# Performance work log

Measured on AMD Instinct MI355X. Metric: run time of the kernel, lower is better.

The kernel has to match this reference:

```python
import jax, jax.numpy as jnp
import numpy as np

B, T, C = 64, 256, 384
H, D = 6, 64  # num_heads, head_size

def setup_inputs() -> dict:
    key = jax.random.key(0)
    ks = jax.random.split(key, 6)
    s = 0.02
    return {
        "x": jax.random.normal(ks[0], (B, T, C), dtype=jnp.float32),
        "Wq": jax.random.normal(ks[1], (H, C, D), dtype=jnp.float32) * s,
        "Wk": jax.random.normal(ks[2], (H, C, D), dtype=jnp.float32) * s,
        "Wv": jax.random.normal(ks[3], (H, C, D), dtype=jnp.float32) * s,
        "Wp": jax.random.normal(ks[4], (C, C), dtype=jnp.float32) * s,
        "bp": jnp.zeros((C,), dtype=jnp.float32),
    }

def reference(x, Wq, Wk, Wv, Wp, bp):
    # per-head projections: [B,T,C] x [H,C,D] -> [B,H,T,D]
    q = jnp.einsum('btc,hcd->bhtd', x, Wq)
    k = jnp.einsum('btc,hcd->bhtd', x, Wk)
    v = jnp.einsum('btc,hcd->bhtd', x, Wv)
    scale = 1.0 / jnp.sqrt(jnp.float32(D))
    scores = jnp.einsum('bhtd,bhsd->bhts', q, k) * scale  # [B,H,T,T]
    Tlen = x.shape[1]
    causal = jnp.tril(jnp.ones((Tlen, Tlen), dtype=bool))
    scores = jnp.where(causal, scores, -jnp.inf)
    wei = jax.nn.softmax(scores, axis=-1)
    # dropout is identity in eval mode
    out = jnp.einsum('bhts,bhsd->bhtd', wei, v)  # [B,H,T,D]
    # concat heads in order (matches torch.cat over head list)
    out = jnp.transpose(out, (0, 2, 1, 3)).reshape(x.shape[0], Tlen, H * D)
    return out @ Wp.T + bp  # nn.Linear: y = x W^T + b
```

## Files before the change

### kernel.cpp

```cpp
#include <hip/hip_runtime.h>

constexpr int Bn = 64, T = 256, C = 384, H = 6, D = 64;
constexpr int BT = Bn * T;
constexpr int NQKV = 3 * C;
constexpr int WALL_ELEMS = NQKV * C;
constexpr int WP_ELEMS = C * C;

using f32x4 = __attribute__((ext_vector_type(4))) float;
using fvec4 = __attribute__((ext_vector_type(4))) float;
using us4   = __attribute__((ext_vector_type(4))) unsigned short;
using us8   = __attribute__((ext_vector_type(8))) unsigned short;
using bf8   = __attribute__((ext_vector_type(8))) __bf16;

__device__ __forceinline__ unsigned short f2bf(float f) {
  unsigned u = __builtin_bit_cast(unsigned, f);
  u += 0x7FFFu + ((u >> 16) & 1u);
  return (unsigned short)(u >> 16);
}

__device__ __forceinline__ f32x4 mfma16(us8 a, us8 b, f32x4 c) {
  return __builtin_amdgcn_mfma_f32_16x16x32_bf16(
      __builtin_bit_cast(bf8, a), __builtin_bit_cast(bf8, b), c, 0, 0, 0);
}

__device__ __forceinline__ void glds16(const unsigned short* g,
                                       unsigned short* l) {
  __builtin_amdgcn_global_load_lds(
      (const __attribute__((address_space(1))) unsigned int*)g,
      (__attribute__((address_space(3))) unsigned int*)l, 16, 0, 0);
}

__global__ __launch_bounds__(256) void k_prep(
    const float* __restrict__ x,
    const float* __restrict__ Wq, const float* __restrict__ Wk,
    const float* __restrict__ Wv, const float* __restrict__ Wp,
    unsigned short* __restrict__ Wall, unsigned short* __restrict__ Wpb,
    unsigned short* __restrict__ Xb) {
  __shared__ unsigned short t[64][71];
  const int bid = blockIdx.x;
  const int tid = threadIdx.x;
  if (bid < 108) {
    const int ct = bid % 6, ph = bid / 6;
    const int h = ph % 6, p = ph / 6;
    const float* W = (p == 0) ? Wq : (p == 1) ? Wk : Wv;
    const int c0 = ct * 64;
    const int d = tid & 63, cq = tid >> 6;
#pragma unroll
    for (int s = 0; s < 16; ++s) {
      const int c_loc = cq * 16 + s;
      t[c_loc][d] = f2bf(W[(size_t)(h * C + c0 + c_loc) * D + d]);
    }
    __syncthreads();
    const int d_loc = tid >> 2, ch = tid & 3;
#pragma unroll
    for (int it = 0; it < 2; ++it) {
      const int cc = (ch + it * 4) * 8;
      us8 o;
#pragma unroll
      for (int j = 0; j < 8; ++j) o[j] = t[cc + j][d_loc];
      *(us8*)&Wall[(size_t)(p * C + h * D + d_loc) * C + c0 + cc] = o;
    }
  } else {
    const float* src;
    unsigned short* dst;
    int off;
    if (bid < 180) { src = Wp; dst = Wpb; off = (bid - 108) * 2048 + tid * 8; }
    else           { src = x;  dst = Xb;  off = (bid - 180) * 2048 + tid * 8; }
    fvec4 a = *(const fvec4*)(src + off);
    fvec4 b = *(const fvec4*)(src + off + 4);
    us8 o;
#pragma unroll
    for (int j = 0; j < 4; ++j) { o[j] = f2bf(a[j]); o[4 + j] = f2bf(b[j]); }
    *(us8*)(dst + off) = o;
  }
}

__device__ __forceinline__ void stage_tile(
    const unsigned short* __restrict__ g, unsigned short* l,
    int row0g, int k0, int tr, int tc, int w) {
#pragma unroll
  for (int s = 0; s < 4; ++s) {
    const int row = s * 32 + tr;
    const int sc = (tc ^ (row & 7)) * 8;
    glds16(g + (size_t)(row0g + row) * C + k0 + sc,
           l + (s * 32 + w * 8) * 64);
  }
}

template <int MODE>
__global__ __launch_bounds__(256) void k_gemm(
    const unsigned short* __restrict__ A, const unsigned short* __restrict__ Bm,
    const float* __restrict__ bias, unsigned short* __restrict__ QKV,
    unsigned short* __restrict__ VT, float* __restrict__ Of, int nwgn) {
  constexpr int BK = 64, NT = C / BK;
  __shared__ unsigned short Al[2][128 * BK];
  __shared__ unsigned short Bl[2][128 * BK];
  const int nwg = gridDim.x;
  const int bid = blockIdx.x;
  const int lin = (bid & 7) * (nwg >> 3) + (bid >> 3);
  const int m0 = (lin / nwgn) * 128, n0 = (lin % nwgn) * 128;
  const int tid = threadIdx.x;
  const int w = tid >> 6, lane = tid & 63;
  const int lr = lane & 15, lg = lane >> 4;
  const int wm = (w >> 1) * 64, wn = (w & 1) * 64;
  const int tr = tid >> 3, tc = tid & 7;

  f32x4 acc[4][4];
#pragma unroll
  for (int i = 0; i < 4; ++i)
#pragma unroll
    for (int j = 0; j < 4; ++j) acc[i][j] = (f32x4){0.f, 0.f, 0.f, 0.f};

  stage_tile(A, &Al[0][0], m0, 0, tr, tc, w);
  stage_tile(Bm, &Bl[0][0], n0, 0, tr, tc, w);
  stage_tile(A, &Al[1][0], m0, BK, tr, tc, w);
  stage_tile(Bm, &Bl[1][0], n0, BK, tr, tc, w);

  int cur = 0;
  for (int t = 0; t < NT; ++t) {
    if (t < NT - 1) {
      asm volatile("s_waitcnt vmcnt(8)" ::: "memory");
    } else {
      asm volatile("s_waitcnt vmcnt(0)" ::: "memory");
    }
    asm volatile("s_barrier" ::: "memory");
#pragma unroll
    for (int kc = 0; kc < 2; ++kc) {
      us8 af[4], bfr[4];
#pragma unroll
      for (int i = 0; i < 4; ++i) {
        const int ra = wm + i * 16 + lr;
        af[i] = *(const us8*)&Al[cur][ra * 64 + (((kc * 4 + lg) ^ (ra & 7)) * 8)];
        const int rb = wn + i * 16 + lr;
        bfr[i] = *(const us8*)&Bl[cur][rb * 64 + (((kc * 4 + lg) ^ (rb & 7)) * 8)];
      }
      __builtin_amdgcn_s_setprio(1);
#pragma unroll
      for (int i = 0; i < 4; ++i)
#pragma unroll
        for (int j = 0; j < 4; ++j)
          acc[i][j] = mfma16(af[i], bfr[j], acc[i][j]);
      __builtin_amdgcn_s_setprio(0);
    }
    asm volatile("s_barrier" ::: "memory");
    if (t + 2 < NT) {
      stage_tile(A, &Al[cur][0], m0, (t + 2) * BK, tr, tc, w);
      stage_tile(Bm, &Bl[cur][0], n0, (t + 2) * BK, tr, tc, w);
    }
    cur ^= 1;
  }

  if (MODE == 1) {
#pragma unroll
    for (int i = 0; i < 4; ++i)
#pragma unroll
      for (int j = 0; j < 4; ++j) {
        const int col = n0 + wn + j * 16 + lr;
        const float bv = bias[col];
#pragma unroll
        for (int r = 0; r < 4; ++r) {
          const size_t row = m0 + wm + i * 16 + lg * 4 + r;
          Of[row * C + col] = acc[i][j][r] + bv;
        }
      }
  } else if (n0 < 2 * C) {
#pragma unroll
    for (int i = 0; i < 4; ++i)
#pragma unroll
      for (int j = 0; j < 4; ++j) {
        const int col = n0 + wn + j * 16 + lr;
#pragma unroll
        for (int r = 0; r < 4; ++r) {
          const size_t row = m0 + wm + i * 16 + lg * 4 + r;
          QKV[row * NQKV + col] = f2bf(acc[i][j][r]);
        }
      }
  } else {
#pragma unroll
    for (int i = 0; i < 4; ++i)
#pragma unroll
      for (int j = 0; j < 4; ++j) {
        const int vcol = n0 + wn + j * 16 + lr - 2 * C;
        const int h = vcol >> 6, d = vcol & 63;
        const int row0 = m0 + wm + i * 16 + lg * 4;
        const int b = row0 >> 8, tq = row0 & 255;
        us4 o4;
#pragma unroll
        for (int r = 0; r < 4; ++r) o4[r] = f2bf(acc[i][j][r]);
        *(us4*)&VT[(((size_t)b * H + h) * D + d) * T + tq] = o4;
      }
  }
}

__global__ __launch_bounds__(512, 4) void k_attn(
    const unsigned short* __restrict__ QKV, const unsigned short* __restrict__ VT,
    unsigned short* __restrict__ Y) {
  __shared__ unsigned short Klds[256][64];
  __shared__ unsigned short Vl[64][256];
  __shared__ unsigned short Pch[8][16][32];
  const int bid = blockIdx.x;
  const int lin = (bid & 7) * 96 + (bid >> 3);
  const int b = lin / 12, rr = lin % 12;
  const int h = rr >> 1, qt = rr & 1;
  const int t0 = qt * 128;
  const int kvlen = t0 + 128;
  const int tid = threadIdx.x;
  const int w = tid >> 6, lane = tid & 63;
  const int lr = lane & 15, lg = lane >> 4;

  const size_t qbase = (size_t)(b * T + t0 + w * 16 + lr) * NQKV + h * D;
  const us8 aq0 = *(const us8*)(QKV + qbase + lg * 8);
  const us8 aq1 = *(const us8*)(QKV + qbase + 32 + lg * 8);
  asm volatile("" ::: "memory");

  {
    const int rl = lane >> 3, cl = lane & 7;
    for (int r0 = 0; r0 < kvlen; r0 += 64) {
      const int row = r0 + w * 8 + rl;
      glds16(QKV + (size_t)(b * T + row) * NQKV + C + h * D +
                 ((cl ^ (row & 7)) * 8),
             &Klds[r0 + w * 8][0]);
    }
    const unsigned short* vbase = VT + ((size_t)b * H + h) * D * T;
    const int dl = lane >> 5, cv = lane & 31;
#pragma unroll
    for (int it = 0; it < 4; ++it) {
      const int d = it * 16 + w * 2 + dl;
      glds16(vbase + (size_t)d * T + ((cv ^ (d & 7)) * 8),
             &Vl[it * 16 + w * 2][0]);
    }
  }
  asm volatile("s_waitcnt vmcnt(4)" ::: "memory");
  asm volatile("s_barrier" ::: "memory");

  const int nsf = kvlen / 16;
  const int xk = lr & 7;

  f32x4 s[16];
#pragma unroll
  for (int sf = 0; sf < 16; ++sf) s[sf] = (f32x4){0.f, 0.f, 0.f, 0.f};
  __builtin_amdgcn_s_setprio(1);
#pragma unroll
  for (int sf = 0; sf < 16; ++sf) {
    if (sf < nsf) {
      us8 kb0 = *(const us8*)&Klds[sf * 16 + lr][(lg ^ xk) * 8];
      s[sf] = mfma16(aq0, kb0, s[sf]);
      us8 kb1 = *(const us8*)&Klds[sf * 16 + lr][((4 + lg) ^ xk) * 8];
      s[sf] = mfma16(aq1, kb1, s[sf]);
    }
  }
  __builtin_amdgcn_s_setprio(0);

  float mrow[4] = {-1e30f, -1e30f, -1e30f, -1e30f};
#pragma unroll
  for (int sf = 0; sf < 16; ++sf) {
    if (sf < nsf) {
#pragma unroll
      for (int r = 0; r < 4; ++r) {
        const int trow = t0 + w * 16 + lg * 4 + r;
        const int scol = sf * 16 + lr;
        float v = s[sf][r] * 0.125f;
        if (scol > trow) v = -1e30f;
        s[sf][r] = v;
        mrow[r] = fmaxf(mrow[r], v);
      }
    }
  }
#pragma unroll
  for (int dd = 1; dd < 16; dd <<= 1)
#pragma unroll
    for (int r = 0; r < 4; ++r)
      mrow[r] = fmaxf(mrow[r], __shfl_xor(mrow[r], dd, 64));

  float psum[4] = {0.f, 0.f, 0.f, 0.f};
#pragma unroll
  for (int sf = 0; sf < 16; ++sf) {
    if (sf < nsf) {
#pragma unroll
      for (int r = 0; r < 4; ++r) {
        float p = __expf(s[sf][r] - mrow[r]);
        s[sf][r] = p;
        psum[r] += p;
      }
    }
  }
#pragma unroll
  for (int dd = 1; dd < 16; dd <<= 1)
#pragma unroll
    for (int r = 0; r < 4; ++r)
      psum[r] += __shfl_xor(psum[r], dd, 64);

  asm volatile("s_waitcnt vmcnt(0)" ::: "memory");
  asm volatile("s_barrier" ::: "memory");

  f32x4 o[4];
#pragma unroll
  for (int nf = 0; nf < 4; ++nf) o[nf] = (f32x4){0.f, 0.f, 0.f, 0.f};
  const int nkk = nsf >> 1;
#pragma unroll
  for (int kk = 0; kk < 8; ++kk) {
    if (kk < nkk) {
#pragma unroll
      for (int half = 0; half < 2; ++half) {
        const int sf = kk * 2 + half;
        const int row = lg * 4;
#pragma unroll
        for (int r = 0; r < 4; ++r) {
          const int cch = (half * 2 + (lr >> 3)) ^ ((row + r) & 3);
          Pch[w][row + r][cch * 8 + (lr & 7)] = f2bf(s[sf][r]);
        }
      }
      __builtin_amdgcn_wave_barrier();
      us8 pa = *(const us8*)&Pch[w][lr][(lg ^ (lr & 3)) * 8];
      __builtin_amdgcn_wave_barrier();
      __builtin_amdgcn_s_setprio(1);
#pragma unroll
      for (int nf = 0; nf < 4; ++nf) {
        us8 bv = *(const us8*)&Vl[nf * 16 + lr][((kk * 4 + lg) ^ xk) * 8];
        o[nf] = mfma16(pa, bv, o[nf]);
      }
      __builtin_amdgcn_s_setprio(0);
    }
  }

  float rs[4];
#pragma unroll
  for (int r = 0; r < 4; ++r) rs[r] = 1.0f / psum[r];
#pragma unroll
  for (int nf = 0; nf < 4; ++nf)
#pragma unroll
    for (int r = 0; r < 4; ++r) {
      const int trow = t0 + w * 16 + lg * 4 + r;
      Y[(size_t)(b * T + trow) * C + h * D + nf * 16 + lr] =
          f2bf(o[nf][r] * rs[r]);
    }
}

extern "C" void kernel_launch(void* const* d_in, const int* in_sizes, int n_in,
                              void* d_out, int out_size, void* d_ws, size_t ws_size,
                              hipStream_t stream) {
  const float* x  = (const float*)d_in[0];
  const float* Wq = (const float*)d_in[1];
  const float* Wk = (const float*)d_in[2];
  const float* Wv = (const float*)d_in[3];
  const float* Wp = (const float*)d_in[4];
  const float* bp = (const float*)d_in[5];
  float* out = (float*)d_out;

  unsigned short* Wall = (unsigned short*)d_ws;
  unsigned short* Wpb  = Wall + WALL_ELEMS;
  unsigned short* QKV  = Wpb + WP_ELEMS;
  unsigned short* Yb   = QKV + (size_t)BT * NQKV;
  unsigned short* VT   = Yb + (size_t)BT * C;
  unsigned short* Xb   = Yb;

  k_prep<<<180 + BT * C / 2048, 256, 0, stream>>>(x, Wq, Wk, Wv, Wp,
                                                  Wall, Wpb, Xb);
  k_gemm<0><<<NQKV / 128 * (BT / 128), 256, 0, stream>>>(
      Xb, Wall, nullptr, QKV, VT, nullptr, NQKV / 128);
  k_attn<<<T / 128 * H * Bn, 512, 0, stream>>>(QKV, VT, Yb);
  k_gemm<1><<<C / 128 * (BT / 128), 256, 0, stream>>>(
      Yb, Wpb, bp, nullptr, nullptr, out, C / 128);
}
```

Before: 69.11 us.

## Split attention KV into two tiles with online softmax and overlapped loads

```diff
diff --git a/kernel.cpp b/kernel.cpp
--- a/kernel.cpp
+++ b/kernel.cpp
@@ -134,13 +134,11 @@
         const int rb = wn + i * 16 + lr;
         bfr[i] = *(const us8*)&Bl[cur][rb * 64 + (((kc * 4 + lg) ^ (rb & 7)) * 8)];
       }
-      __builtin_amdgcn_s_setprio(1);
 #pragma unroll
       for (int i = 0; i < 4; ++i)
 #pragma unroll
         for (int j = 0; j < 4; ++j)
           acc[i][j] = mfma16(af[i], bfr[j], acc[i][j]);
-      __builtin_amdgcn_s_setprio(0);
     }
     asm volatile("s_barrier" ::: "memory");
     if (t + 2 < NT) {
@@ -195,111 +193,115 @@
 __global__ __launch_bounds__(512, 4) void k_attn(
     const unsigned short* __restrict__ QKV, const unsigned short* __restrict__ VT,
     unsigned short* __restrict__ Y) {
-  __shared__ unsigned short Klds[256][64];
-  __shared__ unsigned short Vl[64][256];
+  __shared__ unsigned short Kl[2][128][64];
+  __shared__ unsigned short Vl[2][64][128];
   __shared__ unsigned short Pch[8][16][32];
   const int bid = blockIdx.x;
   const int lin = (bid & 7) * 96 + (bid >> 3);
   const int b = lin / 12, rr = lin % 12;
   const int h = rr >> 1, qt = rr & 1;
   const int t0 = qt * 128;
-  const int kvlen = t0 + 128;
+  const int nt = qt + 1;
   const int tid = threadIdx.x;
   const int w = tid >> 6, lane = tid & 63;
   const int lr = lane & 15, lg = lane >> 4;
+  const int xk = lr & 7;
 
   const size_t qbase = (size_t)(b * T + t0 + w * 16 + lr) * NQKV + h * D;
   const us8 aq0 = *(const us8*)(QKV + qbase + lg * 8);
   const us8 aq1 = *(const us8*)(QKV + qbase + 32 + lg * 8);
   asm volatile("" ::: "memory");
 
-  {
-    const int rl = lane >> 3, cl = lane & 7;
-    for (int r0 = 0; r0 < kvlen; r0 += 64) {
-      const int row = r0 + w * 8 + rl;
-      glds16(QKV + (size_t)(b * T + row) * NQKV + C + h * D +
-                 ((cl ^ (row & 7)) * 8),
-             &Klds[r0 + w * 8][0]);
-    }
-    const unsigned short* vbase = VT + ((size_t)b * H + h) * D * T;
-    const int dl = lane >> 5, cv = lane & 31;
-#pragma unroll
-    for (int it = 0; it < 4; ++it) {
-      const int d = it * 16 + w * 2 + dl;
-      glds16(vbase + (size_t)d * T + ((cv ^ (d & 7)) * 8),
-             &Vl[it * 16 + w * 2][0]);
-    }
-  }
-  asm volatile("s_waitcnt vmcnt(4)" ::: "memory");
+  const unsigned short* kgbase = QKV + (size_t)(b * T) * NQKV + C + h * D;
+  const unsigned short* vbase = VT + ((size_t)b * H + h) * D * T;
+
+  auto stage_kv = [&](int tt) {
+#pragma unroll
+    for (int s = 0; s < 2; ++s) {
+      const int row = s * 64 + w * 8 + (lane >> 3);
+      glds16(kgbase + (size_t)(tt * 128 + row) * NQKV + ((lane & 7) ^ (row & 7)) * 8,
+             &Kl[tt][s * 64 + w * 8][0]);
+    }
+#pragma unroll
+    for (int s = 0; s < 2; ++s) {
+      const int d = s * 32 + w * 4 + (lane >> 4);
+      glds16(vbase + (size_t)d * T + tt * 128 + (((lane & 15) ^ (d & 7)) * 8),
+             &Vl[tt][s * 32 + w * 4][0]);
+    }
+  };
+
+  stage_kv(0);
+  if (nt == 2) stage_kv(1);
+
+  if (nt == 2) asm volatile("s_waitcnt vmcnt(4)" ::: "memory");
+  else         asm volatile("s_waitcnt vmcnt(0)" ::: "memory");
   asm volatile("s_barrier" ::: "memory");
 
-  const int nsf = kvlen / 16;
-  const int xk = lr & 7;
-
-  f32x4 s[16];
-#pragma unroll
-  for (int sf = 0; sf < 16; ++sf) s[sf] = (f32x4){0.f, 0.f, 0.f, 0.f};
-  __builtin_amdgcn_s_setprio(1);
-#pragma unroll
-  for (int sf = 0; sf < 16; ++sf) {
-    if (sf < nsf) {
-      us8 kb0 = *(const us8*)&Klds[sf * 16 + lr][(lg ^ xk) * 8];
+  float m[4] = {-1e30f, -1e30f, -1e30f, -1e30f};
+  float l[4] = {0.f, 0.f, 0.f, 0.f};
+  f32x4 o[4];
+#pragma unroll
+  for (int nf = 0; nf < 4; ++nf) o[nf] = (f32x4){0.f, 0.f, 0.f, 0.f};
+
+  auto process_tile = [&](int tt) {
+    f32x4 s[8];
+#pragma unroll
+    for (int sf = 0; sf < 8; ++sf) s[sf] = (f32x4){0.f, 0.f, 0.f, 0.f};
+#pragma unroll
+    for (int sf = 0; sf < 8; ++sf) {
+      us8 kb0 = *(const us8*)&Kl[tt][sf * 16 + lr][(lg ^ xk) * 8];
       s[sf] = mfma16(aq0, kb0, s[sf]);
-      us8 kb1 = *(const us8*)&Klds[sf * 16 + lr][((4 + lg) ^ xk) * 8];
+      us8 kb1 = *(const us8*)&Kl[tt][sf * 16 + lr][((4 + lg) ^ xk) * 8];
       s[sf] = mfma16(aq1, kb1, s[sf]);
     }
-  }
-  __builtin_amdgcn_s_setprio(0);
-
-  float mrow[4] = {-1e30f, -1e30f, -1e30f, -1e30f};
-#pragma unroll
-  for (int sf = 0; sf < 16; ++sf) {
-    if (sf < nsf) {
+    float tm[4] = {-1e30f, -1e30f, -1e30f, -1e30f};
+#pragma unroll
+    for (int sf = 0; sf < 8; ++sf) {
 #pragma unroll
       for (int r = 0; r < 4; ++r) {
         const int trow = t0 + w * 16 + lg * 4 + r;
-        const int scol = sf * 16 + lr;
+        const int scol = tt * 128 + sf * 16 + lr;
         float v = s[sf][r] * 0.125f;
         if (scol > trow) v = -1e30f;
         s[sf][r] = v;
-        mrow[r] = fmaxf(mrow[r], v);
-      }
-    }
-  }
-#pragma unroll
-  for (int dd = 1; dd < 16; dd <<= 1)
-#pragma unroll
-    for (int r = 0; r < 4; ++r)
-      mrow[r] = fmaxf(mrow[r], __shfl_xor(mrow[r], dd, 64));
-
-  float psum[4] = {0.f, 0.f, 0.f, 0.f};
-#pragma unroll
-  for (int sf = 0; sf < 16; ++sf) {
-    if (sf < nsf) {
+        tm[r] = fmaxf(tm[r], v);
+      }
+    }
+#pragma unroll
+    for (int dd = 1; dd < 16; dd <<= 1)
+#pragma unroll
+      for (int r = 0; r < 4; ++r)
+        tm[r] = fmaxf(tm[r], __shfl_xor(tm[r], dd, 64));
+    float fac[4];
+#pragma unroll
+    for (int r = 0; r < 4; ++r) {
+      const float mn = fmaxf(m[r], tm[r]);
+      fac[r] = __expf(m[r] - mn);
+      m[r] = mn;
+    }
+    float ts[4] = {0.f, 0.f, 0.f, 0.f};
+#pragma unroll
+    for (int sf = 0; sf < 8; ++sf) {
 #pragma unroll
       for (int r = 0; r < 4; ++r) {
-        float p = __expf(s[sf][r] - mrow[r]);
+        float p = __expf(s[sf][r] - m[r]);
         s[sf][r] = p;
-        psum[r] += p;
-      }
-    }
-  }
-#pragma unroll
-  for (int dd = 1; dd < 16; dd <<= 1)
-#pragma unroll
-    for (int r = 0; r < 4; ++r)
-      psum[r] += __shfl_xor(psum[r], dd, 64);
-
-  asm volatile("s_waitcnt vmcnt(0)" ::: "memory");
-  asm volatile("s_barrier" ::: "memory");
-
-  f32x4 o[4];
-#pragma unroll
-  for (int nf = 0; nf < 4; ++nf) o[nf] = (f32x4){0.f, 0.f, 0.f, 0.f};
-  const int nkk = nsf >> 1;
-#pragma unroll
-  for (int kk = 0; kk < 8; ++kk) {
-    if (kk < nkk) {
+        ts[r] += p;
+      }
+    }
+#pragma unroll
+    for (int dd = 1; dd < 16; dd <<= 1)
+#pragma unroll
+      for (int r = 0; r < 4; ++r)
+        ts[r] += __shfl_xor(ts[r], dd, 64);
+#pragma unroll
+    for (int r = 0; r < 4; ++r) l[r] = l[r] * fac[r] + ts[r];
+#pragma unroll
+    for (int nf = 0; nf < 4; ++nf)
+#pragma unroll
+      for (int r = 0; r < 4; ++r) o[nf][r] *= fac[r];
+#pragma unroll
+    for (int kk = 0; kk < 4; ++kk) {
 #pragma unroll
       for (int half = 0; half < 2; ++half) {
         const int sf = kk * 2 + half;
@@ -313,19 +315,24 @@
       __builtin_amdgcn_wave_barrier();
       us8 pa = *(const us8*)&Pch[w][lr][(lg ^ (lr & 3)) * 8];
       __builtin_amdgcn_wave_barrier();
-      __builtin_amdgcn_s_setprio(1);
 #pragma unroll
       for (int nf = 0; nf < 4; ++nf) {
-        us8 bv = *(const us8*)&Vl[nf * 16 + lr][((kk * 4 + lg) ^ xk) * 8];
+        us8 bv = *(const us8*)&Vl[tt][nf * 16 + lr][((kk * 4 + lg) ^ xk) * 8];
         o[nf] = mfma16(pa, bv, o[nf]);
       }
-      __builtin_amdgcn_s_setprio(0);
-    }
+    }
+  };
+
+  process_tile(0);
+  if (nt == 2) {
+    asm volatile("s_waitcnt vmcnt(0)" ::: "memory");
+    asm volatile("s_barrier" ::: "memory");
+    process_tile(1);
   }
 
   float rs[4];
 #pragma unroll
-  for (int r = 0; r < 4; ++r) rs[r] = 1.0f / psum[r];
+  for (int r = 0; r < 4; ++r) rs[r] = 1.0f / l[r];
 #pragma unroll
   for (int nf = 0; nf < 4; ++nf)
 #pragma unroll
```

Measured after the change: 67.45 us. 2.4% less time.
